# Kernel optimization log

Measured on AMD Instinct MI355X. Metric: run time of the kernel, lower is better.

## Reference

```python
import jax, jax.numpy as jnp
import numpy as np

E, K, CAP = 8, 2, 48
RD, NC = 64, 10
LOAD_PEN, MIN_USE, TEMP = 2.0, 0.05, 1.0


def _conv(x, w):
    return jax.lax.conv_general_dilated(x, w, (1, 1), 'SAME',
                                        dimension_numbers=('NCHW', 'OIHW', 'NCHW'))


def _bn(x, g, b):
    # eval-mode BatchNorm2d with running_mean=0, running_var=1, eps=1e-5
    s = g / np.float32(np.sqrt(1.0 + 1e-5))
    return x * s[:, None, None] + b[:, None, None]


def _maxpool2(x):
    return jax.lax.reduce_window(x, -jnp.inf, jax.lax.max,
                                 (1, 1, 2, 2), (1, 1, 2, 2), 'VALID')


def setup_inputs() -> dict:
    key = jax.random.key(0)
    ks = iter(jax.random.split(key, 40))
    n = lambda shape, s=0.1: jax.random.normal(next(ks), shape, jnp.float32) * s
    B = 256
    return dict(
        x=jax.random.normal(next(ks), (B, 3, 32, 32), jnp.float32),
        # routing trunk
        tw1=n((32, 3, 3, 3)), tg1=jnp.ones(32), tb1=jnp.zeros(32),
        tw2=n((32, 32, 3, 3)), tg2=jnp.ones(32), tb2=jnp.zeros(32),
        tfw=n((RD, 128)), tfb=jnp.zeros(RD),
        # gate MLP
        gw1=n((RD // 2, RD)), gb1=jnp.zeros(RD // 2),
        gw2=n((E, RD // 2)), gb2=jnp.zeros(E),
        # per-expert feature extractors (stacked over E)
        ew1=n((E, 32, 3, 3, 3)), eg1=jnp.ones((E, 32)), eb1=jnp.zeros((E, 32)),
        ew2=n((E, 64, 32, 3, 3)), eg2=jnp.ones((E, 64)), eb2=jnp.zeros((E, 64)),
        ew3=n((E, 128, 64, 3, 3)), eg3=jnp.ones((E, 128)), eb3=jnp.zeros((E, 128)),
        efw=n((E, 128, 128)), efb=jnp.zeros((E, 128)),
        # per-expert classifiers (stacked over E)
        cw1=n((E, 64, 128)), cb1=jnp.zeros((E, 64)),
        cw2=n((E, NC, 64)), cb2=jnp.zeros((E, NC)),
    )


def _forward(x, tw1, tg1, tb1, tw2, tg2, tb2, tfw, tfb, gw1, gb1, gw2, gb2,
             ew1, eg1, eb1, ew2, eg2, eb2, ew3, eg3, eb3, efw, efb,
             cw1, cb1, cw2, cb2):
    B = x.shape[0]
    # ---- routing trunk ----
    h = jax.nn.relu(_bn(_conv(x, tw1), tg1, tb1))
    h = jax.nn.relu(_bn(_conv(h, tw2), tg2, tb2))
    h = _maxpool2(h)                                   # [B,32,16,16]
    h = h.reshape(B, 32, 2, 8, 2, 8).mean((3, 5))      # AdaptiveAvgPool2d(2)
    rf = jax.nn.relu(h.reshape(B, 128) @ tfw.T + tfb)  # [B,RD]
    # ---- gate ----
    scores = (jax.nn.relu(rf @ gw1.T + gb1) @ gw2.T + gb2) / TEMP  # [B,E]
    usage = jnp.ones(E, jnp.float32) / E               # expert_usage_ema buffer
    boost = jnp.where(usage < MIN_USE, (MIN_USE - usage) * 10.0, 0.0)
    balanced = scores + boost[None] - LOAD_PEN * usage[None]
    # ---- capacity-constrained top-k routing (eval: sample_order = arange) ----
    _, tk = jax.lax.top_k(balanced, K)                 # [B,K] int32

    def step(loads, tki):
        lt = loads[tki]                                # [K] loads of this sample's top-k
        avail = lt < CAP
        idx = jnp.where(jnp.any(avail), jnp.argmax(avail), jnp.argmin(lt))
        chosen = tki[idx]
        return loads.at[chosen].add(1.0), chosen

    _, chosen = jax.lax.scan(step, jnp.zeros(E, jnp.float32), tk)
    D = jax.nn.one_hot(chosen, E, dtype=bool)          # [B,E] dispatch mask

    # ---- experts: run each expert on the full batch, zero out unassigned ----
    def expert(w1, g1, b1, w2, g2, b2, w3, g3, b3, fw, fb, c1w, c1b, c2w, c2b):
        h = _maxpool2(jax.nn.relu(_bn(_conv(x, w1), g1, b1)))   # [B,32,16,16]
        h = _maxpool2(jax.nn.relu(_bn(_conv(h, w2), g2, b2)))   # [B,64,8,8]
        h = jax.nn.relu(_bn(_conv(h, w3), g3, b3)).mean((2, 3)) # GAP -> [B,128]
        f = jax.nn.relu(h @ fw.T + fb)
        return jax.nn.relu(f @ c1w.T + c1b) @ c2w.T + c2b        # [B,NC]

    outs = jax.vmap(expert)(ew1, eg1, eb1, ew2, eg2, eb2, ew3, eg3, eb3,
                            efw, efb, cw1, cb1, cw2, cb2)        # [E,B,NC]
    expert_outputs = jnp.where(D.T[:, :, None], outs, 0.0).transpose(1, 0, 2)  # [B,E,NC]

    # ---- combine via softmax over dispatched scores ----
    masked = jnp.where(D, balanced, -jnp.inf)
    rw = jax.nn.softmax(masked, axis=1) * D
    rw = rw / (rw.sum(1, keepdims=True) + 1e-12)
    final = jnp.einsum('be,bec->bc', rw, expert_outputs)         # [B,NC]
    return final, balanced, D


def reference(x, tw1, tg1, tb1, tw2, tg2, tb2, tfw, tfb, gw1, gb1, gw2, gb2,
              ew1, eg1, eb1, ew2, eg2, eb2, ew3, eg3, eb3, efw, efb,
              cw1, cb1, cw2, cb2):
    return _forward(x, tw1, tg1, tb1, tw2, tg2, tb2, tfw, tfb,
                    gw1, gb1, gw2, gb2, ew1, eg1, eb1, ew2, eg2, eb2,
                    ew3, eg3, eb3, efw, efb, cw1, cb1, cw2, cb2)
```

## Files before the change

kernel.cpp:

```cpp
#include <hip/hip_runtime.h>
#include <hip/hip_bf16.h>
#include <math.h>


#define BN_RS (1.0f / sqrtf(1.00001f))

typedef __attribute__((ext_vector_type(8))) short short8;
typedef __attribute__((ext_vector_type(4))) float floatx4;

static __device__ __forceinline__ ushort f2bf(float f) {
  unsigned u = __float_as_uint(f);
  unsigned r = (u + 0x7fffu + ((u >> 16) & 1u)) >> 16;
  return (ushort)r;
}
static __device__ __forceinline__ float bf2f(ushort h) {
  return __uint_as_float((unsigned)h << 16);
}

#define WS_TFP    0
#define WS_TK     262144
#define WS_W2H    264192
#define WS_W2L    282624
#define WS_EW2B   301056
#define WS_EW3B   595968

__global__ __launch_bounds__(256) void prep_kernel(
    const float* __restrict__ tw2, const float* __restrict__ ew2,
    const float* __restrict__ ew3, ushort* __restrict__ w2h,
    ushort* __restrict__ w2l, ushort* __restrict__ ew2b,
    ushort* __restrict__ ew3b)
{
  const int j = blockIdx.x * 256 + threadIdx.x;
  if (j < 9216) {
    int tap = j >> 10, oc = (j >> 5) & 31, ic = j & 31;
    float v = tw2[oc*288 + ic*9 + tap];
    ushort h = f2bf(v);
    w2h[j] = h;
    w2l[j] = f2bf(v - bf2f(h));
  } else if (j < 156672) {
    int jj = j - 9216;
    int e = jj / 18432, r2 = jj % 18432;
    int tap = r2 / 2048, r3 = r2 % 2048;
    int oc = r3 / 32, ic = r3 % 32;
    ew2b[jj] = f2bf(ew2[e*18432 + oc*288 + ic*9 + tap]);
  } else if (j < 746496) {
    int jj = j - 156672;
    int e = jj / 73728, r2 = jj % 73728;
    int tap = r2 / 8192, r3 = r2 % 8192;
    int oc = r3 / 64, ic = r3 % 64;
    ew3b[jj] = f2bf(ew3[e*73728 + oc*576 + ic*9 + tap]);
  }
}

__global__ __launch_bounds__(256, 2) void trunk_kernel(
    const float* __restrict__ x, const float* __restrict__ tw1,
    const float* __restrict__ tg1, const float* __restrict__ tb1,
    const ushort* __restrict__ w2h, const ushort* __restrict__ w2l,
    const float* __restrict__ tg2, const float* __restrict__ tb2,
    float* __restrict__ tfp)
{
  __shared__ __align__(16) ushort smu[31648];
  float* smf = (float*)&smu[27200];
  const int t = threadIdx.x;
  const int b = blockIdx.x >> 2, rs = blockIdx.x & 3;
  const int r0 = rs * 8;

  {
    uint4 z = {0, 0, 0, 0};
    for (int j = t; j < 3400; j += 256) ((uint4*)smu)[j] = z;
  }
  for (int j = t; j < 1296; j += 256) {
    int ic = j / 432, rem = j % 432, rr = rem / 36, c = rem % 36;
    int gy = r0 - 2 + rr, gx = c - 1;
    float v = 0.f;
    if (gy >= 0 && gy < 32 && gx >= 0 && gx < 32)
      v = x[b*3072 + ic*1024 + gy*32 + gx];
    smf[j] = v;
  }
  for (int j = t; j < 864; j += 256) {
    int oc = j / 27, r = j % 27, ic = r / 9, k = r % 9;
    smf[1296 + ic*288 + k*32 + oc] = tw1[j];
  }
  if (t < 32) { smf[2160 + t] = tg1[t]*BN_RS; smf[2160 + 32 + t] = tb1[t]; }
  __syncthreads();

  for (int it = 0; it < 2; ++it) {
    const int item = it*256 + t;
    if (item < 320) {
      const int g2 = item & 15, chf = (item >> 4) & 1, rr = item >> 5;
      const int grow = r0 - 1 + rr;
      if (grow >= 0 && grow < 32) {
        const int c0 = chf * 16;
        float acc[2][16];
        #pragma unroll
        for (int c = 0; c < 16; ++c) { acc[0][c] = 0.f; acc[1][c] = 0.f; }
        for (int ic = 0; ic < 3; ++ic) {
          float wa[9], wb[9];
          #pragma unroll
          for (int k = 0; k < 9; ++k) {
            float2 wv = *(const float2*)&smf[1296 + ic*288 + k*32 + 2*g2];
            wa[k] = wv.x; wb[k] = wv.y;
          }
          #pragma unroll
          for (int ky = 0; ky < 3; ++ky) {
            const float* srow = &smf[ic*432 + (rr + ky)*36 + c0];
            float v[18];
            #pragma unroll
            for (int j4 = 0; j4 < 4; ++j4) {
              float4 q = *(const float4*)&srow[4*j4];
              v[4*j4] = q.x; v[4*j4+1] = q.y; v[4*j4+2] = q.z; v[4*j4+3] = q.w;
            }
            v[16] = srow[16]; v[17] = srow[17];
            #pragma unroll
            for (int kx = 0; kx < 3; ++kx) {
              const float fa = wa[ky*3+kx], fb = wb[ky*3+kx];
              #pragma unroll
              for (int c = 0; c < 16; ++c) {
                acc[0][c] = fmaf(fa, v[c+kx], acc[0][c]);
                acc[1][c] = fmaf(fb, v[c+kx], acc[1][c]);
              }
            }
          }
        }
        const float sa = smf[2160 + 2*g2],     ba = smf[2160 + 32 + 2*g2];
        const float sb = smf[2160 + 2*g2 + 1], bb = smf[2160 + 32 + 2*g2 + 1];
        uint* imgH32 = (uint*)smu;
        uint* imgL32 = (uint*)(smu + 13600);
        #pragma unroll
        for (int c = 0; c < 16; ++c) {
          float va = fmaxf(fmaf(acc[0][c], sa, ba), 0.f);
          float vb = fmaxf(fmaf(acc[1][c], sb, bb), 0.f);
          ushort ha = f2bf(va), hb = f2bf(vb);
          ushort la = f2bf(va - bf2f(ha)), lb = f2bf(vb - bf2f(hb));
          const int u = (rr*34 + c0 + c + 1)*20 + g2;
          imgH32[u] = (uint)ha | ((uint)hb << 16);
          imgL32[u] = (uint)la | ((uint)lb << 16);
        }
      }
    }
  }
  __syncthreads();

  const int w8 = t >> 6, l = t & 63, col = l & 15, quad = l >> 4;
  const int xh = w8 >> 1, nt = w8 & 1;
  floatx4 acc2[8];
  #pragma unroll
  for (int y = 0; y < 8; ++y)
    #pragma unroll
    for (int i = 0; i < 4; ++i) acc2[y][i] = 0.f;

  #pragma unroll
  for (int dx = 0; dx < 3; ++dx) {
    short8 ah[10], al[10];
    #pragma unroll
    for (int r = 0; r < 10; ++r) {
      const int idx = (r*34 + xh*16 + col + dx)*40 + quad*8;
      ah[r] = *(const short8*)&smu[idx];
      al[r] = *(const short8*)&smu[13600 + idx];
    }
    #pragma unroll
    for (int dy = 0; dy < 3; ++dy) {
      const int wi = (dy*3 + dx)*1024 + (nt*16 + col)*32 + quad*8;
      short8 bh = *(const short8*)&w2h[wi];
      short8 bl = *(const short8*)&w2l[wi];
      #pragma unroll
      for (int y = 0; y < 8; ++y) {
        acc2[y] = __builtin_amdgcn_mfma_f32_16x16x32_bf16(ah[y+dy], bh, acc2[y], 0, 0, 0);
        acc2[y] = __builtin_amdgcn_mfma_f32_16x16x32_bf16(ah[y+dy], bl, acc2[y], 0, 0, 0);
        acc2[y] = __builtin_amdgcn_mfma_f32_16x16x32_bf16(al[y+dy], bh, acc2[y], 0, 0, 0);
      }
    }
  }

  {
    const int oc = nt*16 + col;
    const float s2 = tg2[oc]*BN_RS, bo2 = tb2[oc];
    float psum = 0.f;
    #pragma unroll
    for (int yp = 0; yp < 4; ++yp)
      #pragma unroll
      for (int i2 = 0; i2 < 2; ++i2) {
        float v00 = fmaxf(fmaf(acc2[2*yp][2*i2],     s2, bo2), 0.f);
        float v01 = fmaxf(fmaf(acc2[2*yp][2*i2+1],   s2, bo2), 0.f);
        float v10 = fmaxf(fmaf(acc2[2*yp+1][2*i2],   s2, bo2), 0.f);
        float v11 = fmaxf(fmaf(acc2[2*yp+1][2*i2+1], s2, bo2), 0.f);
        psum += fmaxf(fmaxf(v00, v01), fmaxf(v10, v11));
      }
    psum += __shfl_xor(psum, 16);
    psum += __shfl_xor(psum, 32);
    if (quad == 0) tfp[b*256 + (rs*2 + xh)*32 + oc] = psum;
  }
}

__global__ __launch_bounds__(64) void gate_kernel(
    const float* __restrict__ tfp, const float* __restrict__ tfw, const float* __restrict__ tfb,
    const float* __restrict__ gw1, const float* __restrict__ gb1,
    const float* __restrict__ gw2, const float* __restrict__ gb2,
    float* __restrict__ outBal, int* __restrict__ tk)
{
  __shared__ float feat[128], rf[64], g1[32], bal[8];
  const int b = blockIdx.x, t = threadIdx.x;
  #pragma unroll
  for (int h = 0; h < 2; ++h) {
    const int f = t + 64*h;
    const int oc = f >> 2, qy = (f >> 1) & 1, qx = f & 1;
    feat[f] = (tfp[b*256 + (4*qy + qx)*32 + oc] +
               tfp[b*256 + (4*qy + 2 + qx)*32 + oc]) * (1.f/64.f);
  }
  __syncthreads();
  {
    float a = tfb[t];
    const float4* wp = (const float4*)&tfw[t*128];
    #pragma unroll 8
    for (int i4 = 0; i4 < 32; ++i4) {
      float4 wv = wp[i4];
      a = fmaf(wv.x, feat[4*i4], a);   a = fmaf(wv.y, feat[4*i4+1], a);
      a = fmaf(wv.z, feat[4*i4+2], a); a = fmaf(wv.w, feat[4*i4+3], a);
    }
    rf[t] = fmaxf(a, 0.f);
  }
  __syncthreads();
  if (t < 32) {
    float a = gb1[t];
    const float4* wp = (const float4*)&gw1[t*64];
    #pragma unroll
    for (int i4 = 0; i4 < 16; ++i4) {
      float4 wv = wp[i4];
      a = fmaf(wv.x, rf[4*i4], a);   a = fmaf(wv.y, rf[4*i4+1], a);
      a = fmaf(wv.z, rf[4*i4+2], a); a = fmaf(wv.w, rf[4*i4+3], a);
    }
    g1[t] = fmaxf(a, 0.f);
  }
  __syncthreads();
  if (t < 8) {
    float a = gb2[t];
    const float4* wp = (const float4*)&gw2[t*32];
    #pragma unroll
    for (int i4 = 0; i4 < 8; ++i4) {
      float4 wv = wp[i4];
      a = fmaf(wv.x, g1[4*i4], a);   a = fmaf(wv.y, g1[4*i4+1], a);
      a = fmaf(wv.z, g1[4*i4+2], a); a = fmaf(wv.w, g1[4*i4+3], a);
    }
    const float v = a - 0.25f;
    bal[t] = v;
    outBal[b*8 + t] = v;
  }
  __syncthreads();
  if (t == 0) {
    int t0 = 0; float b0 = bal[0];
    #pragma unroll
    for (int e2 = 1; e2 < 8; ++e2) if (bal[e2] > b0) { b0 = bal[e2]; t0 = e2; }
    int t1 = -1; float b1 = -3.4e38f;
    #pragma unroll
    for (int e2 = 0; e2 < 8; ++e2) if (e2 != t0 && bal[e2] > b1) { b1 = bal[e2]; t1 = e2; }
    tk[b*2] = t0; tk[b*2 + 1] = t1;
  }
}

#define XA_IMG  0
#define XA_FEAT 3600
#define XA_SFF  3728
#define XA_SGG  3856
#define XA_XF   9040
#define XA_W1F  12508
#define XA_BN1F 13372
#define XA_SC   9040
__global__ __launch_bounds__(512, 2) void expALL_kernel(
    const float* __restrict__ x, const int* __restrict__ tk,
    const float* __restrict__ ew1, const float* __restrict__ eg1,
    const float* __restrict__ eb1, const ushort* __restrict__ ew2b,
    const float* __restrict__ eg2, const float* __restrict__ eb2,
    const ushort* __restrict__ ew3b, const float* __restrict__ eg3,
    const float* __restrict__ eb3, const float* __restrict__ efw,
    const float* __restrict__ efb, const float* __restrict__ cw1,
    const float* __restrict__ cb1, const float* __restrict__ cw2,
    const float* __restrict__ cb2, float* __restrict__ outF,
    float* __restrict__ outD)
{
  __shared__ __align__(16) ushort smu[27296];
  __shared__ int stk[512];
  __shared__ int sch;
  float* smf = (float*)smu;
  const int t = threadIdx.x, b = blockIdx.x;
  const int w8 = t >> 6, l = t & 63;
  const int col = l & 15, quad = l >> 4;

  stk[t] = tk[t];
  __syncthreads();
  if (t == 0) {
    unsigned long long Lp = 0ull;
    int chv = 0;
    for (int i = 0; i <= b; ++i) {
      const int a = stk[2*i], c = stk[2*i+1];
      const int la = (int)((Lp >> (a*8)) & 0xFFull);
      const int lc = (int)((Lp >> (c*8)) & 0xFFull);
      chv = (la < 48) ? a : ((lc < 48) ? c : ((la <= lc) ? a : c));
      Lp += 1ull << (chv*8);
    }
    sch = chv;
  } else {
    uint4 z; z.x = 0; z.y = 0; z.z = 0; z.w = 0;
    for (int j = t-1; j < 1620; j += 511) ((uint4*)smu)[j] = z;
    for (int j = t-1; j < 3468; j += 511) {
      int ic = j / 1156, rem = j % 1156, p = rem / 34, cpd = rem % 34;
      int gy = p - 1, gx = cpd - 1;
      float v = 0.f;
      if (gy >= 0 && gy < 32 && gx >= 0 && gx < 32) v = x[b*3072 + ic*1024 + gy*32 + gx];
      smf[XA_XF + j] = v;
    }
  }
  __syncthreads();
  const int e = sch;
  if (t < 8) outD[b*8 + t] = (t == e) ? 1.f : 0.f;

  const int ntile = w8 & 3, mhalf = w8 >> 2;
  short8 w2f[9];
  {
    const int oc2 = ntile*16 + col;
    #pragma unroll
    for (int tap = 0; tap < 9; ++tap)
      w2f[tap] = *(const short8*)&ew2b[(e*9 + tap)*2048 + oc2*32 + quad*8];
  }

  for (int j = t; j < 864; j += 512) {
    int oc = j / 27, r = j % 27, ic = r / 9, k = r % 9;
    smf[XA_W1F + ic*288 + k*32 + oc] = ew1[e*864 + j];
  }
  if (t < 32) { smf[XA_BN1F + t] = eg1[e*32 + t]*BN_RS; smf[XA_BN1F + 32 + t] = eb1[e*32 + t]; }
  __syncthreads();

  {
    const int g = t >> 5, c = t & 31;
    for (int rs = 0; rs < 4; ++rs) {
      const int r0 = rs * 8;
      float acc[2][8];
      #pragma unroll
      for (int o = 0; o < 2; ++o)
        #pragma unroll
        for (int r = 0; r < 8; ++r) acc[o][r] = 0.f;
      for (int ic = 0; ic < 3; ++ic) {
        float w[2][9];
        #pragma unroll
        for (int k = 0; k < 9; ++k) {
          float2 wv = *(const float2*)&smf[XA_W1F + ic*288 + k*32 + 2*g];
          w[0][k] = wv.x; w[1][k] = wv.y;
        }
        const float* src = &smf[XA_XF + ic*1156 + r0*34 + c];
        #pragma unroll
        for (int rr = 0; rr < 10; ++rr) {
          const float i0 = src[rr*34], i1 = src[rr*34 + 1], i2 = src[rr*34 + 2];
          #pragma unroll
          for (int dr = 0; dr < 3; ++dr) {
            const int r = rr - dr;
            if (r < 0 || r > 7) continue;
            #pragma unroll
            for (int o = 0; o < 2; ++o) {
              acc[o][r] = fmaf(w[o][dr*3+0], i0, acc[o][r]);
              acc[o][r] = fmaf(w[o][dr*3+1], i1, acc[o][r]);
              acc[o][r] = fmaf(w[o][dr*3+2], i2, acc[o][r]);
            }
          }
        }
      }
      #pragma unroll
      for (int o = 0; o < 2; ++o) {
        const int oc = 2*g + o;
        const float s = smf[XA_BN1F + oc], bo = smf[XA_BN1F + 32 + oc];
        float m[4];
        #pragma unroll
        for (int pr = 0; pr < 4; ++pr) {
          float v0 = fmaxf(fmaf(acc[o][2*pr],   s, bo), 0.f);
          float v1 = fmaxf(fmaf(acc[o][2*pr+1], s, bo), 0.f);
          m[pr] = fmaxf(v0, v1);
        }
        #pragma unroll
        for (int pr = 0; pr < 4; ++pr) {
          float nb = __shfl_xor(m[pr], 1);
          m[pr] = fmaxf(m[pr], nb);
        }
        if (!(c & 1)) {
          const int pc = c >> 1;
          #pragma unroll
          for (int pr = 0; pr < 4; ++pr)
            smu[XA_IMG + ((rs*4 + pr + 1)*18 + (pc + 1))*40 + oc] = f2bf(m[pr]);
        }
      }
    }
  }
  __syncthreads();

  const int oc3 = w8*16 + col;
  short8 w3f[9][2];
  #pragma unroll
  for (int tap = 0; tap < 9; ++tap)
    #pragma unroll
    for (int ks = 0; ks < 2; ++ks)
      w3f[tap][ks] = *(const short8*)&ew3b[(e*9 + tap)*8192 + oc3*64 + ks*32 + quad*8];

  {
    floatx4 acc[8];
    #pragma unroll
    for (int mt = 0; mt < 8; ++mt)
      #pragma unroll
      for (int i = 0; i < 4; ++i) acc[mt][i] = 0.f;

    #pragma unroll
    for (int tap = 0; tap < 9; ++tap) {
      const int dy = tap / 3, dx = tap % 3;
      #pragma unroll
      for (int mtl = 0; mtl < 8; ++mtl) {
        const int mt = mhalf*8 + mtl;
        short8 afr = *(const short8*)
            &smu[XA_IMG + ((mt + dy)*18 + col + dx)*40 + quad*8];
        acc[mtl] = __builtin_amdgcn_mfma_f32_16x16x32_bf16(afr, w2f[tap], acc[mtl], 0, 0, 0);
      }
    }
    __syncthreads();

    {
      uint4 z; z.x = 0; z.y = 0; z.z = 0; z.w = 0;
      for (int j = t; j < 288; j += 512) {
        int slot = j >> 3, ofs = (j & 7) * 8, row, cl;
        if (slot < 10)      { row = 0; cl = slot; }
        else if (slot < 20) { row = 9; cl = slot - 10; }
        else if (slot < 28) { row = 1 + (slot - 20); cl = 0; }
        else                { row = 1 + (slot - 28); cl = 9; }
        *(uint4*)&smu[(row*10 + cl)*72 + ofs] = z;
      }
    }
    const int oc2 = ntile*16 + col;
    const float s2 = eg2[e*64 + oc2]*BN_RS, bo2 = eb2[e*64 + oc2];
    #pragma unroll
    for (int mtpl = 0; mtpl < 4; ++mtpl) {
      const int mtp = mhalf*4 + mtpl;
      float a00 = fmaxf(fmaf(acc[2*mtpl][0],   s2, bo2), 0.f);
      float a01 = fmaxf(fmaf(acc[2*mtpl][1],   s2, bo2), 0.f);
      float a02 = fmaxf(fmaf(acc[2*mtpl][2],   s2, bo2), 0.f);
      float a03 = fmaxf(fmaf(acc[2*mtpl][3],   s2, bo2), 0.f);
      float a10 = fmaxf(fmaf(acc[2*mtpl+1][0], s2, bo2), 0.f);
      float a11 = fmaxf(fmaf(acc[2*mtpl+1][1], s2, bo2), 0.f);
      float a12 = fmaxf(fmaf(acc[2*mtpl+1][2], s2, bo2), 0.f);
      float a13 = fmaxf(fmaf(acc[2*mtpl+1][3], s2, bo2), 0.f);
      float p0 = fmaxf(fmaxf(a00, a01), fmaxf(a10, a11));
      float p1 = fmaxf(fmaxf(a02, a03), fmaxf(a12, a13));
      smu[((mtp + 1)*10 + (quad*2 + 1))*72 + oc2] = f2bf(p0);
      smu[((mtp + 1)*10 + (quad*2 + 2))*72 + oc2] = f2bf(p1);
    }
  }
  __syncthreads();

  const int fcout = t & 127, fcpart = t >> 7;
  float4 efr[8];
  {
    const float4* wp = (const float4*)&efw[e*16384 + fcout*128 + fcpart*32];
    #pragma unroll
    for (int i4 = 0; i4 < 8; ++i4) efr[i4] = wp[i4];
  }

  {
    floatx4 acc[4];
    #pragma unroll
    for (int mt = 0; mt < 4; ++mt)
      #pragma unroll
      for (int i = 0; i < 4; ++i) acc[mt][i] = 0.f;

    #pragma unroll
    for (int tap = 0; tap < 9; ++tap) {
      const int dy = tap / 3, dx = tap % 3;
      #pragma unroll
      for (int ks = 0; ks < 2; ++ks) {
        #pragma unroll
        for (int mt = 0; mt < 4; ++mt) {
          const int m = mt*16 + col;
          const int y = m >> 3, xx = m & 7;
          short8 afr = *(const short8*)
              &smu[((y + dy)*10 + (xx + dx))*72 + ks*32 + quad*8];
          acc[mt] = __builtin_amdgcn_mfma_f32_16x16x32_bf16(afr, w3f[tap][ks], acc[mt], 0, 0, 0);
        }
      }
    }

    {
      const float s = eg3[e*128 + oc3]*BN_RS, bo = eb3[e*128 + oc3];
      float gsum = 0.f;
      #pragma unroll
      for (int mt = 0; mt < 4; ++mt)
        #pragma unroll
        for (int i = 0; i < 4; ++i)
          gsum += fmaxf(fmaf(acc[mt][i], s, bo), 0.f);
      gsum += __shfl_xor(gsum, 16);
      gsum += __shfl_xor(gsum, 32);
      if (quad == 0) smf[XA_FEAT + oc3] = gsum * (1.f/64.f);
    }
  }
  __syncthreads();

  {
    float a = (fcpart == 0) ? efb[e*128 + fcout] : 0.f;
    #pragma unroll
    for (int i4 = 0; i4 < 8; ++i4) {
      float4 wv = efr[i4];
      const int base = XA_FEAT + fcpart*32 + 4*i4;
      a = fmaf(wv.x, smf[base], a);     a = fmaf(wv.y, smf[base + 1], a);
      a = fmaf(wv.z, smf[base + 2], a); a = fmaf(wv.w, smf[base + 3], a);
    }
    smf[XA_SC + fcpart*128 + fcout] = a;
  }
  __syncthreads();
  if (t < 128)
    smf[XA_SFF + t] = fmaxf(smf[XA_SC + t] + smf[XA_SC + 128 + t] +
                            smf[XA_SC + 256 + t] + smf[XA_SC + 384 + t], 0.f);
  __syncthreads();
  if (t < 256) {
    const int out = t & 63, part = t >> 6;
    float a = (part == 0) ? cb1[e*64 + out] : 0.f;
    const float4* wp = (const float4*)&cw1[e*8192 + out*128 + part*32];
    #pragma unroll
    for (int i4 = 0; i4 < 8; ++i4) {
      float4 wv = wp[i4];
      const int base = XA_SFF + part*32 + 4*i4;
      a = fmaf(wv.x, smf[base], a);     a = fmaf(wv.y, smf[base + 1], a);
      a = fmaf(wv.z, smf[base + 2], a); a = fmaf(wv.w, smf[base + 3], a);
    }
    smf[XA_SC + part*64 + out] = a;
  }
  __syncthreads();
  if (t < 64)
    smf[XA_SGG + t] = fmaxf(smf[XA_SC + t] + smf[XA_SC + 64 + t] +
                            smf[XA_SC + 128 + t] + smf[XA_SC + 192 + t], 0.f);
  __syncthreads();
  if (t < 10) {
    float a = cb2[e*10 + t];
    const float4* wp = (const float4*)&cw2[e*640 + t*64];
    #pragma unroll
    for (int i4 = 0; i4 < 16; ++i4) {
      float4 wv = wp[i4];
      a = fmaf(wv.x, smf[XA_SGG + 4*i4],     a);
      a = fmaf(wv.y, smf[XA_SGG + 4*i4 + 1], a);
      a = fmaf(wv.z, smf[XA_SGG + 4*i4 + 2], a);
      a = fmaf(wv.w, smf[XA_SGG + 4*i4 + 3], a);
    }
    outF[b*10 + t] = a;
  }
}

extern "C" void kernel_launch(void* const* d_in, const int* in_sizes, int n_in,
                              void* d_out, int out_size, void* d_ws, size_t ws_size,
                              hipStream_t stream)
{
  const float* x   = (const float*)d_in[0];
  const float* tw1 = (const float*)d_in[1];
  const float* tg1 = (const float*)d_in[2];
  const float* tb1 = (const float*)d_in[3];
  const float* tw2 = (const float*)d_in[4];
  const float* tg2 = (const float*)d_in[5];
  const float* tb2 = (const float*)d_in[6];
  const float* tfw = (const float*)d_in[7];
  const float* tfb = (const float*)d_in[8];
  const float* gw1 = (const float*)d_in[9];
  const float* gb1 = (const float*)d_in[10];
  const float* gw2 = (const float*)d_in[11];
  const float* gb2 = (const float*)d_in[12];
  const float* ew1 = (const float*)d_in[13];
  const float* eg1 = (const float*)d_in[14];
  const float* eb1 = (const float*)d_in[15];
  const float* ew2 = (const float*)d_in[16];
  const float* eg2 = (const float*)d_in[17];
  const float* eb2 = (const float*)d_in[18];
  const float* ew3 = (const float*)d_in[19];
  const float* eg3 = (const float*)d_in[20];
  const float* eb3 = (const float*)d_in[21];
  const float* efw = (const float*)d_in[22];
  const float* efb = (const float*)d_in[23];
  const float* cw1 = (const float*)d_in[24];
  const float* cb1 = (const float*)d_in[25];
  const float* cw2 = (const float*)d_in[26];
  const float* cb2 = (const float*)d_in[27];

  float*  out  = (float*)d_out;
  char*   ws   = (char*)d_ws;
  float*  tfp  = (float*)(ws + WS_TFP);
  int*    tk   = (int*)(ws + WS_TK);
  ushort* w2h  = (ushort*)(ws + WS_W2H);
  ushort* w2l  = (ushort*)(ws + WS_W2L);
  ushort* ew2b = (ushort*)(ws + WS_EW2B);
  ushort* ew3b = (ushort*)(ws + WS_EW3B);

  prep_kernel<<<2916, 256, 0, stream>>>(tw2, ew2, ew3, w2h, w2l, ew2b, ew3b);
  trunk_kernel<<<1024, 256, 0, stream>>>(x, tw1, tg1, tb1, w2h, w2l, tg2, tb2, tfp);
  gate_kernel<<<256, 64, 0, stream>>>(tfp, tfw, tfb, gw1, gb1, gw2, gb2,
                                      out + 2560, tk);
  expALL_kernel<<<256, 512, 0, stream>>>(x, tk, ew1, eg1, eb1, ew2b, eg2, eb2,
                                         ew3b, eg3, eb3, efw, efb, cw1, cb1,
                                         cw2, cb2, out, out + 4608);
}
```

Measured before the change: 182.9 us.

## Split trunk conv tiles by column half and vectorize weight prep conversion

The trunk kernel now assigns each block an 8-row by 16-column tile instead of an 8-row full-width tile. This doubles the grid to 2048 blocks and roughly halves shared memory per block, allowing four blocks per CU. The price is recomputing halo columns in the first conv and an extra cross-wave reduction through shared memory with a sync. Separately, the prep kernel converts eight expert conv weights per thread and writes them as one short8 vector, cutting its grid from 2916 to 396 blocks.

New measurement: 287.0 us. 1.57x slower.

```diff
diff --git a/kernel.cpp b/kernel.cpp
--- a/kernel.cpp
+++ b/kernel.cpp
@@ -37,41 +37,49 @@
     ushort h = f2bf(v);
     w2h[j] = h;
     w2l[j] = f2bf(v - bf2f(h));
-  } else if (j < 156672) {
-    int jj = j - 9216;
+  } else if (j < 27648) {
+    const int jj = (j - 9216) * 8;
     int e = jj / 18432, r2 = jj % 18432;
     int tap = r2 / 2048, r3 = r2 % 2048;
-    int oc = r3 / 32, ic = r3 % 32;
-    ew2b[jj] = f2bf(ew2[e*18432 + oc*288 + ic*9 + tap]);
-  } else if (j < 746496) {
-    int jj = j - 156672;
+    int oc = r3 / 32, ic0 = r3 % 32;
+    const float* src = &ew2[e*18432 + oc*288 + ic0*9 + tap];
+    short8 o;
+    #pragma unroll
+    for (int k = 0; k < 8; ++k) o[k] = (short)f2bf(src[k*9]);
+    *(short8*)&ew2b[jj] = o;
+  } else if (j < 101376) {
+    const int jj = (j - 27648) * 8;
     int e = jj / 73728, r2 = jj % 73728;
     int tap = r2 / 8192, r3 = r2 % 8192;
-    int oc = r3 / 64, ic = r3 % 64;
-    ew3b[jj] = f2bf(ew3[e*73728 + oc*576 + ic*9 + tap]);
+    int oc = r3 / 64, ic0 = r3 % 64;
+    const float* src = &ew3[e*73728 + oc*576 + ic0*9 + tap];
+    short8 o;
+    #pragma unroll
+    for (int k = 0; k < 8; ++k) o[k] = (short)f2bf(src[k*9]);
+    *(short8*)&ew3b[jj] = o;
   }
 }
 
-__global__ __launch_bounds__(256, 2) void trunk_kernel(
+__global__ __launch_bounds__(256, 4) void trunk_kernel(
     const float* __restrict__ x, const float* __restrict__ tw1,
     const float* __restrict__ tg1, const float* __restrict__ tb1,
     const ushort* __restrict__ w2h, const ushort* __restrict__ w2l,
     const float* __restrict__ tg2, const float* __restrict__ tb2,
     float* __restrict__ tfp)
 {
-  __shared__ __align__(16) ushort smu[31648];
-  float* smf = (float*)&smu[27200];
-  const int t = threadIdx.x;
-  const int b = blockIdx.x >> 2, rs = blockIdx.x & 3;
-  const int r0 = rs * 8;
+  __shared__ __align__(16) ushort smu[17696];
+  float* smf = (float*)&smu[14400];
+  const int t = threadIdx.x, blk = blockIdx.x;
+  const int b = blk >> 3, rs = (blk >> 1) & 3, ch = blk & 1;
+  const int r0 = rs * 8, c0 = ch * 16;
 
   {
     uint4 z = {0, 0, 0, 0};
-    for (int j = t; j < 3400; j += 256) ((uint4*)smu)[j] = z;
-  }
-  for (int j = t; j < 1296; j += 256) {
-    int ic = j / 432, rem = j % 432, rr = rem / 36, c = rem % 36;
-    int gy = r0 - 2 + rr, gx = c - 1;
+    for (int j = t; j < 1800; j += 256) ((uint4*)smu)[j] = z;
+  }
+  for (int j = t; j < 720; j += 256) {
+    int ic = j / 240, rem = j % 240, rr = rem / 20, c = rem % 20;
+    int gy = r0 - 2 + rr, gx = c0 - 2 + c;
     float v = 0.f;
     if (gy >= 0 && gy < 32 && gx >= 0 && gx < 32)
       v = x[b*3072 + ic*1024 + gy*32 + gx];
@@ -79,84 +87,83 @@
   }
   for (int j = t; j < 864; j += 256) {
     int oc = j / 27, r = j % 27, ic = r / 9, k = r % 9;
-    smf[1296 + ic*288 + k*32 + oc] = tw1[j];
-  }
-  if (t < 32) { smf[2160 + t] = tg1[t]*BN_RS; smf[2160 + 32 + t] = tb1[t]; }
-  __syncthreads();
-
-  for (int it = 0; it < 2; ++it) {
-    const int item = it*256 + t;
-    if (item < 320) {
-      const int g2 = item & 15, chf = (item >> 4) & 1, rr = item >> 5;
-      const int grow = r0 - 1 + rr;
-      if (grow >= 0 && grow < 32) {
-        const int c0 = chf * 16;
-        float acc[2][16];
-        #pragma unroll
-        for (int c = 0; c < 16; ++c) { acc[0][c] = 0.f; acc[1][c] = 0.f; }
-        for (int ic = 0; ic < 3; ++ic) {
-          float wa[9], wb[9];
+    smf[720 + ic*288 + k*32 + oc] = tw1[j];
+  }
+  if (t < 32) { smf[1584 + t] = tg1[t]*BN_RS; smf[1584 + 32 + t] = tb1[t]; }
+  __syncthreads();
+
+  if (t < 160) {
+    const int g2 = t & 15, rr = t >> 4;
+    const int grow = r0 - 1 + rr;
+    if (grow >= 0 && grow < 32) {
+      float acc[2][18];
+      #pragma unroll
+      for (int c = 0; c < 18; ++c) { acc[0][c] = 0.f; acc[1][c] = 0.f; }
+      for (int ic = 0; ic < 3; ++ic) {
+        float wa[9], wb[9];
+        #pragma unroll
+        for (int k = 0; k < 9; ++k) {
+          float2 wv = *(const float2*)&smf[720 + ic*288 + k*32 + 2*g2];
+          wa[k] = wv.x; wb[k] = wv.y;
+        }
+        #pragma unroll
+        for (int ky = 0; ky < 3; ++ky) {
+          const float* srow = &smf[ic*240 + (rr + ky)*20];
+          float v[20];
           #pragma unroll
-          for (int k = 0; k < 9; ++k) {
-            float2 wv = *(const float2*)&smf[1296 + ic*288 + k*32 + 2*g2];
-            wa[k] = wv.x; wb[k] = wv.y;
+          for (int j4 = 0; j4 < 5; ++j4) {
+            float4 q = *(const float4*)&srow[4*j4];
+            v[4*j4] = q.x; v[4*j4+1] = q.y; v[4*j4+2] = q.z; v[4*j4+3] = q.w;
           }
           #pragma unroll
-          for (int ky = 0; ky < 3; ++ky) {
-            const float* srow = &smf[ic*432 + (rr + ky)*36 + c0];
-            float v[18];
+          for (int kx = 0; kx < 3; ++kx) {
+            const float fa = wa[ky*3+kx], fb = wb[ky*3+kx];
             #pragma unroll
-            for (int j4 = 0; j4 < 4; ++j4) {
-              float4 q = *(const float4*)&srow[4*j4];
-              v[4*j4] = q.x; v[4*j4+1] = q.y; v[4*j4+2] = q.z; v[4*j4+3] = q.w;
-            }
-            v[16] = srow[16]; v[17] = srow[17];
-            #pragma unroll
-            for (int kx = 0; kx < 3; ++kx) {
-              const float fa = wa[ky*3+kx], fb = wb[ky*3+kx];
-              #pragma unroll
-              for (int c = 0; c < 16; ++c) {
-                acc[0][c] = fmaf(fa, v[c+kx], acc[0][c]);
-                acc[1][c] = fmaf(fb, v[c+kx], acc[1][c]);
-              }
+            for (int c = 0; c < 18; ++c) {
+              acc[0][c] = fmaf(fa, v[c+kx], acc[0][c]);
+              acc[1][c] = fmaf(fb, v[c+kx], acc[1][c]);
             }
           }
         }
-        const float sa = smf[2160 + 2*g2],     ba = smf[2160 + 32 + 2*g2];
-        const float sb = smf[2160 + 2*g2 + 1], bb = smf[2160 + 32 + 2*g2 + 1];
-        uint* imgH32 = (uint*)smu;
-        uint* imgL32 = (uint*)(smu + 13600);
-        #pragma unroll
-        for (int c = 0; c < 16; ++c) {
-          float va = fmaxf(fmaf(acc[0][c], sa, ba), 0.f);
-          float vb = fmaxf(fmaf(acc[1][c], sb, bb), 0.f);
-          ushort ha = f2bf(va), hb = f2bf(vb);
-          ushort la = f2bf(va - bf2f(ha)), lb = f2bf(vb - bf2f(hb));
-          const int u = (rr*34 + c0 + c + 1)*20 + g2;
-          imgH32[u] = (uint)ha | ((uint)hb << 16);
-          imgL32[u] = (uint)la | ((uint)lb << 16);
-        }
-      }
-    }
-  }
-  __syncthreads();
-
-  const int w8 = t >> 6, l = t & 63, col = l & 15, quad = l >> 4;
-  const int xh = w8 >> 1, nt = w8 & 1;
-  floatx4 acc2[8];
+      }
+      const float sa = smf[1584 + 2*g2],     ba = smf[1584 + 32 + 2*g2];
+      const float sb = smf[1584 + 2*g2 + 1], bb = smf[1584 + 32 + 2*g2 + 1];
+      uint* imgH32 = (uint*)smu;
+      uint* imgL32 = (uint*)(smu + 7200);
+      #pragma unroll
+      for (int c = 0; c < 18; ++c) {
+        const int gcol = c0 - 1 + c;
+        float va = 0.f, vb = 0.f;
+        if (gcol >= 0 && gcol < 32) {
+          va = fmaxf(fmaf(acc[0][c], sa, ba), 0.f);
+          vb = fmaxf(fmaf(acc[1][c], sb, bb), 0.f);
+        }
+        ushort ha = f2bf(va), hb = f2bf(vb);
+        ushort la = f2bf(va - bf2f(ha)), lb = f2bf(vb - bf2f(hb));
+        const int u = (rr*18 + c)*20 + g2;
+        imgH32[u] = (uint)ha | ((uint)hb << 16);
+        imgL32[u] = (uint)la | ((uint)lb << 16);
+      }
+    }
+  }
+  __syncthreads();
+
+  const int w4 = t >> 6, l = t & 63, col = l & 15, quad = l >> 4;
+  const int nt = w4 & 1, yh = w4 >> 1;
+  floatx4 acc2[4];
   #pragma unroll
-  for (int y = 0; y < 8; ++y)
+  for (int y = 0; y < 4; ++y)
     #pragma unroll
     for (int i = 0; i < 4; ++i) acc2[y][i] = 0.f;
 
   #pragma unroll
   for (int dx = 0; dx < 3; ++dx) {
-    short8 ah[10], al[10];
-    #pragma unroll
-    for (int r = 0; r < 10; ++r) {
-      const int idx = (r*34 + xh*16 + col + dx)*40 + quad*8;
-      ah[r] = *(const short8*)&smu[idx];
-      al[r] = *(const short8*)&smu[13600 + idx];
+    short8 ah[6], al[6];
+    #pragma unroll
+    for (int k = 0; k < 6; ++k) {
+      const int idx = ((yh*4 + k)*18 + col + dx)*40 + quad*8;
+      ah[k] = *(const short8*)&smu[idx];
+      al[k] = *(const short8*)&smu[7200 + idx];
     }
     #pragma unroll
     for (int dy = 0; dy < 3; ++dy) {
@@ -164,7 +171,7 @@
       short8 bh = *(const short8*)&w2h[wi];
       short8 bl = *(const short8*)&w2l[wi];
       #pragma unroll
-      for (int y = 0; y < 8; ++y) {
+      for (int y = 0; y < 4; ++y) {
         acc2[y] = __builtin_amdgcn_mfma_f32_16x16x32_bf16(ah[y+dy], bh, acc2[y], 0, 0, 0);
         acc2[y] = __builtin_amdgcn_mfma_f32_16x16x32_bf16(ah[y+dy], bl, acc2[y], 0, 0, 0);
         acc2[y] = __builtin_amdgcn_mfma_f32_16x16x32_bf16(al[y+dy], bh, acc2[y], 0, 0, 0);
@@ -177,7 +184,7 @@
     const float s2 = tg2[oc]*BN_RS, bo2 = tb2[oc];
     float psum = 0.f;
     #pragma unroll
-    for (int yp = 0; yp < 4; ++yp)
+    for (int yp = 0; yp < 2; ++yp)
       #pragma unroll
       for (int i2 = 0; i2 < 2; ++i2) {
         float v00 = fmaxf(fmaf(acc2[2*yp][2*i2],     s2, bo2), 0.f);
@@ -188,7 +195,12 @@
       }
     psum += __shfl_xor(psum, 16);
     psum += __shfl_xor(psum, 32);
-    if (quad == 0) tfp[b*256 + (rs*2 + xh)*32 + oc] = psum;
+    if (yh == 1 && quad == 0) smf[nt*32 + col] = psum;
+    __syncthreads();
+    if (yh == 0 && quad == 0) {
+      float tot = psum + smf[nt*32 + col];
+      tfp[b*256 + (rs*2 + ch)*32 + oc] = tot;
+    }
   }
 }
 
@@ -586,8 +598,8 @@
   ushort* ew2b = (ushort*)(ws + WS_EW2B);
   ushort* ew3b = (ushort*)(ws + WS_EW3B);
 
-  prep_kernel<<<2916, 256, 0, stream>>>(tw2, ew2, ew3, w2h, w2l, ew2b, ew3b);
-  trunk_kernel<<<1024, 256, 0, stream>>>(x, tw1, tg1, tb1, w2h, w2l, tg2, tb2, tfp);
+  prep_kernel<<<396, 256, 0, stream>>>(tw2, ew2, ew3, w2h, w2l, ew2b, ew3b);
+  trunk_kernel<<<2048, 256, 0, stream>>>(x, tw1, tg1, tb1, w2h, w2l, tg2, tb2, tfp);
   gate_kernel<<<256, 64, 0, stream>>>(tfp, tfw, tfb, gw1, gb1, gw2, gb2,
                                       out + 2560, tk);
   expALL_kernel<<<256, 512, 0, stream>>>(x, tk, ew1, eg1, eb1, ew2b, eg2, eb2,
```
